# Kernel optimization log

Hardware: AMD Instinct MI355X
Metric: run time of the kernel (lower is better)

The kernel has to match this reference:

```python
import jax, jax.numpy as jnp
import numpy as np

N, E, F_IN, H, G, A, OUT = 50000, 800000, 128, 256, 64, 8, 1


def _lin(k, fi, fo):
    s = 1.0 / np.sqrt(fi)
    kw, kb = jax.random.split(k)
    W = jax.random.uniform(kw, (fi, fo), jnp.float32, -s, s)
    b = jax.random.uniform(kb, (fo,), jnp.float32, -s, s)
    return W, b


def setup_inputs() -> dict:
    key = jax.random.key(0)
    ks = jax.random.split(key, 12)
    x = jax.random.normal(ks[0], (N, F_IN), jnp.float32)
    edge_index = jax.random.randint(ks[1], (2, E), 0, N, dtype=jnp.int64)
    batch = jnp.sort(jax.random.randint(ks[2], (N,), 0, G, dtype=jnp.int64))
    graph_attr = jax.random.normal(ks[3], (G, A), jnp.float32)
    W1, b1 = _lin(ks[4], F_IN, H)
    W2, b2 = _lin(ks[5], H, H)
    W3, b3 = _lin(ks[6], H, H)
    fcW1, fcb1 = _lin(ks[7], H + A, H)
    fcW2, fcb2 = _lin(ks[8], H, OUT)
    ones = jnp.ones((H,), jnp.float32)
    zeros = jnp.zeros((H,), jnp.float32)
    return dict(x=x, graph_attr=graph_attr, edge_index=edge_index, batch=batch,
                W1=W1, b1=b1, W2=W2, b2=b2, W3=W3, b3=b3,
                g1=ones, be1=zeros, g2=ones, be2=zeros, g3=ones, be3=zeros,
                fcW1=fcW1, fcb1=fcb1, fcW2=fcW2, fcb2=fcb2)


def gcn_conv(x, W, b, src, dst, n):
    # PyG GCNConv: add self-loops, symmetric normalization, xW then scatter-add
    xw = x @ W  # [N, H]
    loop = jnp.arange(n)
    src2 = jnp.concatenate([src, loop])
    dst2 = jnp.concatenate([dst, loop])
    deg = jnp.zeros((n,), xw.dtype).at[dst2].add(1.0)
    dinv = jnp.where(deg > 0, jax.lax.rsqrt(deg), 0.0)
    norm = dinv[src2] * dinv[dst2]  # [E+N]
    out = jnp.zeros((n, xw.shape[1]), xw.dtype).at[dst2].add(xw[src2] * norm[:, None])
    return out + b


def layer_norm(x, g, b, eps=1e-5):
    m = x.mean(-1, keepdims=True)
    v = ((x - m) ** 2).mean(-1, keepdims=True)
    return (x - m) * jax.lax.rsqrt(v + eps) * g + b


def reference(x, graph_attr, edge_index, batch,
              W1, b1, W2, b2, W3, b3,
              g1, be1, g2, be2, g3, be3,
              fcW1, fcb1, fcW2, fcb2):
    src, dst = edge_index[0], edge_index[1]
    h = jax.nn.relu(layer_norm(gcn_conv(x, W1, b1, src, dst, N), g1, be1))
    h = jax.nn.relu(layer_norm(gcn_conv(h, W2, b2, src, dst, N), g2, be2))
    h = jax.nn.relu(layer_norm(gcn_conv(h, W3, b3, src, dst, N), g3, be3))
    # global mean pool over graph ids
    sums = jax.ops.segment_sum(h, batch, num_segments=G)
    cnts = jax.ops.segment_sum(jnp.ones((N,), h.dtype), batch, num_segments=G)
    pooled = sums / jnp.maximum(cnts, 1.0)[:, None]  # [G, H]
    z = jnp.concatenate([pooled, graph_attr.reshape(-1, A)], axis=1)
    z = jax.nn.relu(z @ fcW1 + fcb1)
    return z @ fcW2 + fcb2  # [G, OUT]
```

## Files before the change

kernel.cpp:

```cpp
#include <hip/hip_runtime.h>
#include <hip/hip_bf16.h>

#define N_NODES 50000
#define N_EDGES 800000
#define F_IN    128
#define H_DIM   256
#define G_NUM   64
#define A_DIM   8

typedef __attribute__((ext_vector_type(8))) short short8v;
typedef __attribute__((ext_vector_type(4))) float float4v;
typedef __attribute__((ext_vector_type(2))) float float2v;

__device__ __forceinline__ float b2f(unsigned short u) {
    return __uint_as_float(((unsigned int)u) << 16);
}
__device__ __forceinline__ unsigned short f2b(float v) {
    return __hip_bfloat16_raw(__float2bfloat16(v)).x;
}
__device__ __forceinline__ unsigned char f2fp8(float v) {
    return (unsigned char)(__builtin_amdgcn_cvt_pk_fp8_f32(v, v, 0, false) & 0xff);
}
__device__ __forceinline__ unsigned int pack2(float a, float b) {
    return (unsigned int)f2b(a) | ((unsigned int)f2b(b) << 16);
}
__device__ __forceinline__ void accadd16(float2v* a, uint4 v) {
    a[0] += __builtin_amdgcn_cvt_pk_f32_fp8((int)v.x, false);
    a[1] += __builtin_amdgcn_cvt_pk_f32_fp8((int)v.x, true);
    a[2] += __builtin_amdgcn_cvt_pk_f32_fp8((int)v.y, false);
    a[3] += __builtin_amdgcn_cvt_pk_f32_fp8((int)v.y, true);
    a[4] += __builtin_amdgcn_cvt_pk_f32_fp8((int)v.z, false);
    a[5] += __builtin_amdgcn_cvt_pk_f32_fp8((int)v.z, true);
    a[6] += __builtin_amdgcn_cvt_pk_f32_fp8((int)v.w, false);
    a[7] += __builtin_amdgcn_cvt_pk_f32_fp8((int)v.w, true);
}


__global__ void init_kernel(const int* __restrict__ dst, int* __restrict__ indeg,
                            unsigned short* __restrict__ eloc,
                            const float4* __restrict__ x, uint2* __restrict__ xb,
                            const float* __restrict__ W1, unsigned short* __restrict__ Wt1,
                            const float* __restrict__ W2, unsigned short* __restrict__ Wt2,
                            const float* __restrict__ W3, unsigned short* __restrict__ Wt3) {
    const int EB = (N_EDGES + 255) / 256;
    const int n_x4 = N_NODES * F_IN / 4;
    const int n_w1 = F_IN * H_DIM;
    const int n_w2 = H_DIM * H_DIM;
    int b = blockIdx.x, t = threadIdx.x;
    if (b < EB) {
        int i = b * 256 + t;
        if (i < N_EDGES)
            eloc[i] = (unsigned short)atomicAdd(&indeg[dst[i]], 1);
        return;
    }
    int i = (b - EB) * 256 + t;
    if (i < n_x4) {
        float4 v = x[i];
        uint2 o;
        o.x = pack2(v.x, v.y);
        o.y = pack2(v.z, v.w);
        xb[i] = o;
    } else {
        int j = i - n_x4;
        if (j < n_w1) {
            int k = j / H_DIM, n = j % H_DIM;
            Wt1[(size_t)n * F_IN + k] = f2b(W1[j]);
        } else if (j < n_w1 + n_w2) {
            int j2 = j - n_w1;
            int k = j2 / H_DIM, n = j2 % H_DIM;
            Wt2[(size_t)n * H_DIM + k] = f2b(W2[j2]);
        } else if (j < n_w1 + 2 * n_w2) {
            int j3 = j - n_w1 - n_w2;
            int k = j3 / H_DIM, n = j3 % H_DIM;
            Wt3[(size_t)n * H_DIM + k] = f2b(W3[j3]);
        }
    }
}


__global__ __launch_bounds__(256) void scan1_kernel(const int* __restrict__ in,
                                                    int* __restrict__ out,
                                                    int* __restrict__ bsum,
                                                    float* __restrict__ dinv, int n) {
    __shared__ int tile[256];
    int b = blockIdx.x, t = threadIdx.x, i = b * 256 + t;
    int v = (i < n) ? in[i] : 0;
    if (i < n) dinv[i] = rsqrtf((float)v + 1.0f);
    tile[t] = v;
    __syncthreads();
    #pragma unroll
    for (int o = 1; o < 256; o <<= 1) {
        int add = (t >= o) ? tile[t - o] : 0;
        __syncthreads();
        tile[t] += add;
        __syncthreads();
    }
    if (i < n) out[i] = tile[t] - v;
    if (t == 255) bsum[b] = tile[255];
}

__global__ __launch_bounds__(256) void scan2_kernel(int* __restrict__ bsum, int nb,
                                                    const int* __restrict__ batch,
                                                    int* __restrict__ gstart,
                                                    float* __restrict__ pooled) {
    __shared__ int tile[256];
    int t = threadIdx.x;
    int v = (t < nb) ? bsum[t] : 0;
    tile[t] = v;
    __syncthreads();
    #pragma unroll
    for (int o = 1; o < 256; o <<= 1) {
        int add = (t >= o) ? tile[t - o] : 0;
        __syncthreads();
        tile[t] += add;
        __syncthreads();
    }
    if (t < nb) bsum[t] = tile[t] - v;
    if (t <= G_NUM) {
        int lo = 0, hi = N_NODES;
        while (lo < hi) {
            int mid = (lo + hi) >> 1;
            if (batch[mid] < t) lo = mid + 1; else hi = mid;
        }
        gstart[t] = lo;
    }
    for (int i = t; i < G_NUM * H_DIM; i += 256) pooled[i] = 0.f;
}

__global__ __launch_bounds__(256) void scan3_kernel(int* __restrict__ out,
                                                    const int* __restrict__ bsum, int n) {
    int i = blockIdx.x * blockDim.x + threadIdx.x;
    if (i < n) out[i] = out[i] + bsum[i >> 8];
    if (i == 0) out[n] = N_EDGES;
}


#define SK 40

__device__ __forceinline__ void gemm_body_f8(const unsigned short* __restrict__ A,
                                             const unsigned short* __restrict__ Bt,
                                             unsigned char* __restrict__ C8,
                                             const float* __restrict__ dinv,
                                             int M, int K, int bm) {
    __shared__ unsigned short As[128][SK];
    __shared__ unsigned short Bs[256][SK];
    int t = threadIdx.x;
    int wave = t >> 6, lane = t & 63;
    int wm0 = (wave & 1) * 64, wn0 = (wave >> 1) * 64;
    int l15 = lane & 15, lq = lane >> 4;
    float4v acc[4][4];
    #pragma unroll
    for (int i = 0; i < 4; i++)
        #pragma unroll
        for (int j = 0; j < 4; j++)
            acc[i][j] = (float4v){0.f, 0.f, 0.f, 0.f};

    for (int k0 = 0; k0 < K; k0 += 32) {
        {
            int row = t >> 2, koff = (t & 3) * 8;
            uint4 va = make_uint4(0u, 0u, 0u, 0u);
            if (bm + row < M)
                va = *(const uint4*)(A + (size_t)(bm + row) * K + k0 + koff);
            *(uint4*)&As[row][koff] = va;
        }
        #pragma unroll
        for (int h = 0; h < 2; h++) {
            int c = t + h * 512;
            int row = c >> 2, koff = (c & 3) * 8;
            uint4 vb = *(const uint4*)(Bt + (size_t)row * K + k0 + koff);
            *(uint4*)&Bs[row][koff] = vb;
        }
        __syncthreads();
        short8v af[4], bf[4];
        #pragma unroll
        for (int i = 0; i < 4; i++) {
            af[i] = *(const short8v*)&As[wm0 + i * 16 + l15][lq * 8];
            bf[i] = *(const short8v*)&Bs[wn0 + i * 16 + l15][lq * 8];
        }
        #pragma unroll
        for (int i = 0; i < 4; i++)
            #pragma unroll
            for (int j = 0; j < 4; j++)
                acc[i][j] = __builtin_amdgcn_mfma_f32_16x16x32_bf16(af[i], bf[j], acc[i][j], 0, 0, 0);
        __syncthreads();
    }
    #pragma unroll
    for (int i = 0; i < 4; i++) {
        #pragma unroll
        for (int r = 0; r < 4; r++) {
            int row = bm + wm0 + i * 16 + lq * 4 + r;
            if (row < M) {
                float dv = dinv[row];
                #pragma unroll
                for (int j = 0; j < 4; j++) {
                    int col = wn0 + j * 16 + l15;
                    C8[(size_t)row * H_DIM + col] = f2fp8(dv * acc[i][j][r]);
                }
            }
        }
    }
}

__global__ __launch_bounds__(512) void gemm_f8(const unsigned short* __restrict__ A,
                                               const unsigned short* __restrict__ Bt,
                                               unsigned char* __restrict__ C8,
                                               const float* __restrict__ dinv,
                                               int M, int K) {
    gemm_body_f8(A, Bt, C8, dinv, M, K, blockIdx.x * 128);
}


__global__ __launch_bounds__(512) void fuse1_kernel(const unsigned short* __restrict__ Xb,
                                                    const unsigned short* __restrict__ Wt1,
                                                    unsigned char* __restrict__ P8,
                                                    const float* __restrict__ dinv,
                                                    const int* __restrict__ src,
                                                    const int* __restrict__ dst,
                                                    const unsigned short* __restrict__ eloc,
                                                    const int* __restrict__ rowptr,
                                                    unsigned short* __restrict__ csr_src) {
    const int GB = (N_NODES + 127) / 128;
    int b = blockIdx.x;
    if (b < GB) {
        gemm_body_f8(Xb, Wt1, P8, dinv, N_NODES, F_IN, b * 128);
        return;
    }
    int i = (b - GB) * 512 + threadIdx.x;
    if (i < N_EDGES) {
        int d = dst[i];
        csr_src[rowptr[d] + (int)eloc[i]] = (unsigned short)src[i];
    }
}


template<int F, bool DO_LN>
__global__ __launch_bounds__(256) void gather_ns(const unsigned char* __restrict__ xw,
                                                 unsigned short* __restrict__ out,
                                                 const int* __restrict__ rowptr,
                                                 const unsigned short* __restrict__ csr_src,
                                                 const float* __restrict__ dinv,
                                                 const float* __restrict__ bias,
                                                 const float* __restrict__ gamma,
                                                 const float* __restrict__ beta) {
    constexpr int BPL = F / 16;
    constexpr int NF2 = BPL / 2;
    int lane = threadIdx.x & 63;
    int wave = threadIdx.x >> 6;
    int p = lane & 15;
    int gbase = lane & 48;
    int node = blockIdx.x * 16 + wave * 4 + (lane >> 4);
    int beg = rowptr[node];
    int deg = rowptr[node + 1] - beg;
    const unsigned char* xp = xw + (size_t)p * BPL;

    float2v acc2[NF2];
    #pragma unroll
    for (int k = 0; k < NF2; k++) acc2[k] = (float2v){0.f, 0.f};

    {
        uint4 v = *(const uint4*)(xp + (size_t)node * F);
        accadd16(acc2, v);
    }

    for (int b0 = 0; b0 < deg; b0 += 16) {
        int m = deg - b0; if (m > 16) m = 16;
        int sv = (p < m) ? (int)csr_src[beg + b0 + p] : 0;
        int j = 0;
        for (; j + 4 <= m; j += 4) {
            int s0 = __shfl(sv, gbase | j, 64);
            int s1 = __shfl(sv, gbase | (j + 1), 64);
            int s2 = __shfl(sv, gbase | (j + 2), 64);
            int s3 = __shfl(sv, gbase | (j + 3), 64);
            uint4 v0 = *(const uint4*)(xp + (size_t)s0 * F);
            uint4 v1 = *(const uint4*)(xp + (size_t)s1 * F);
            uint4 v2 = *(const uint4*)(xp + (size_t)s2 * F);
            uint4 v3 = *(const uint4*)(xp + (size_t)s3 * F);
            accadd16(acc2, v0); accadd16(acc2, v1);
            accadd16(acc2, v2); accadd16(acc2, v3);
        }
        for (; j < m; ++j) {
            int s0 = __shfl(sv, gbase | j, 64);
            uint4 v0 = *(const uint4*)(xp + (size_t)s0 * F);
            accadd16(acc2, v0);
        }
    }

    float d = dinv[node];
    float v[BPL];
    #pragma unroll
    for (int k = 0; k < NF2; k++) { v[2 * k] = d * acc2[k].x; v[2 * k + 1] = d * acc2[k].y; }

    if constexpr (DO_LN) {
        #pragma unroll
        for (int q = 0; q < BPL / 4; q++) {
            float4 bi = ((const float4*)bias)[p * (BPL / 4) + q];
            v[q * 4 + 0] += bi.x; v[q * 4 + 1] += bi.y;
            v[q * 4 + 2] += bi.z; v[q * 4 + 3] += bi.w;
        }
        float s = 0.f, ss = 0.f;
        #pragma unroll
        for (int k = 0; k < BPL; k++) { s += v[k]; ss += v[k] * v[k]; }
        #pragma unroll
        for (int o = 1; o < 16; o <<= 1) {
            s  += __shfl_xor(s, o, 64);
            ss += __shfl_xor(ss, o, 64);
        }
        float mn = s * (1.f / F);
        float var = ss * (1.f / F) - mn * mn;
        float rstd = rsqrtf(var + 1e-5f);
        #pragma unroll
        for (int q = 0; q < BPL / 4; q++) {
            float4 ga = ((const float4*)gamma)[p * (BPL / 4) + q];
            float4 be = ((const float4*)beta)[p * (BPL / 4) + q];
            v[q * 4 + 0] = fmaxf((v[q * 4 + 0] - mn) * rstd * ga.x + be.x, 0.f);
            v[q * 4 + 1] = fmaxf((v[q * 4 + 1] - mn) * rstd * ga.y + be.y, 0.f);
            v[q * 4 + 2] = fmaxf((v[q * 4 + 2] - mn) * rstd * ga.z + be.z, 0.f);
            v[q * 4 + 3] = fmaxf((v[q * 4 + 3] - mn) * rstd * ga.w + be.w, 0.f);
        }
    }

    unsigned short* op = out + (size_t)node * F + p * BPL;
    uint4 o0;
    o0.x = pack2(v[0], v[1]); o0.y = pack2(v[2], v[3]);
    o0.z = pack2(v[4], v[5]); o0.w = pack2(v[6], v[7]);
    *(uint4*)op = o0;
    if constexpr (F == 256) {
        uint4 o1;
        o1.x = pack2(v[8],  v[9]);  o1.y = pack2(v[10], v[11]);
        o1.z = pack2(v[12], v[13]); o1.w = pack2(v[14], v[15]);
        *(uint4*)(op + 8) = o1;
    }
}


__global__ __launch_bounds__(128) void pool_kernel(const unsigned int* __restrict__ h32,
                                                   const int* __restrict__ batch,
                                                   float* __restrict__ pooled, int n) {
    int t = threadIdx.x;
    int start = blockIdx.x * 64;
    int end = min(start + 64, n);
    if (start >= n) return;
    int cur = batch[start];
    float a0 = 0.f, a1 = 0.f;
    for (int i = start; i < end; ++i) {
        int g = batch[i];
        if (g != cur) {
            atomicAdd(&pooled[(size_t)cur * H_DIM + 2 * t], a0);
            atomicAdd(&pooled[(size_t)cur * H_DIM + 2 * t + 1], a1);
            a0 = a1 = 0.f;
            cur = g;
        }
        unsigned int u = h32[(size_t)i * (H_DIM / 2) + t];
        a0 += b2f((unsigned short)(u & 0xffffu));
        a1 += b2f((unsigned short)(u >> 16));
    }
    atomicAdd(&pooled[(size_t)cur * H_DIM + 2 * t], a0);
    atomicAdd(&pooled[(size_t)cur * H_DIM + 2 * t + 1], a1);
}


__global__ __launch_bounds__(256) void fc_kernel(const float* __restrict__ pooled,
                                                 const int* __restrict__ gstart,
                                                 const float* __restrict__ gattr,
                                                 const float* __restrict__ fcW1,
                                                 const float* __restrict__ fcb1,
                                                 const float* __restrict__ fcW2,
                                                 const float* __restrict__ fcb2,
                                                 float* __restrict__ out) {
    __shared__ float zc[H_DIM + A_DIM];
    __shared__ float z1[H_DIM];
    int g = blockIdx.x, t = threadIdx.x;
    int c_i = gstart[g + 1] - gstart[g];
    float c = (float)(c_i > 1 ? c_i : 1);
    zc[t] = pooled[(size_t)g * H_DIM + t] / c;
    if (t < A_DIM) zc[H_DIM + t] = gattr[g * A_DIM + t];
    __syncthreads();
    float s = fcb1[t];
    for (int k = 0; k < H_DIM + A_DIM; k++)
        s += zc[k] * fcW1[(size_t)k * H_DIM + t];
    z1[t] = fmaxf(s, 0.f) * fcW2[t];
    __syncthreads();
    for (int off = 128; off; off >>= 1) {
        if (t < off) z1[t] += z1[t + off];
        __syncthreads();
    }
    if (t == 0) out[g] = z1[0] + fcb2[0];
}


extern "C" void kernel_launch(void* const* d_in, const int* in_sizes, int n_in,
                              void* d_out, int out_size, void* d_ws, size_t ws_size,
                              hipStream_t stream) {
    const float* x     = (const float*)d_in[0];
    const float* gattr = (const float*)d_in[1];
    const int*   ei    = (const int*)d_in[2];
    const int*   batch = (const int*)d_in[3];
    const float* W1 = (const float*)d_in[4];  const float* b1 = (const float*)d_in[5];
    const float* W2 = (const float*)d_in[6];  const float* b2 = (const float*)d_in[7];
    const float* W3 = (const float*)d_in[8];  const float* b3 = (const float*)d_in[9];
    const float* g1 = (const float*)d_in[10]; const float* be1 = (const float*)d_in[11];
    const float* g2 = (const float*)d_in[12]; const float* be2 = (const float*)d_in[13];
    const float* g3 = (const float*)d_in[14]; const float* be3 = (const float*)d_in[15];
    const float* fcW1 = (const float*)d_in[16]; const float* fcb1 = (const float*)d_in[17];
    const float* fcW2 = (const float*)d_in[18]; const float* fcb2 = (const float*)d_in[19];
    float* out = (float*)d_out;

    char* w = (char*)d_ws;
    unsigned char*  Pb8 = (unsigned char*)w;  w += (size_t)N_NODES * H_DIM;
    unsigned short* Hb  = (unsigned short*)w; w += (size_t)N_NODES * H_DIM * 2;
    unsigned short* Xb  = (unsigned short*)w; w += (size_t)N_NODES * F_IN * 2;
    unsigned short* Wt1 = (unsigned short*)w; w += (size_t)H_DIM * F_IN * 2;
    unsigned short* Wt2 = (unsigned short*)w; w += (size_t)H_DIM * H_DIM * 2;
    unsigned short* Wt3 = (unsigned short*)w; w += (size_t)H_DIM * H_DIM * 2;
    float* dinv   = (float*)w; w += (size_t)N_NODES * 4;
    float* pooled = (float*)w; w += (size_t)G_NUM * H_DIM * 4;
    int* indeg    = (int*)w;   w += (size_t)N_NODES * 4;
    int* rowptr   = (int*)w;   w += (size_t)(N_NODES + 4) * 4;
    unsigned short* eloc    = (unsigned short*)w; w += (size_t)N_EDGES * 2;
    unsigned short* csr_src = (unsigned short*)w; w += (size_t)N_EDGES * 2;
    int* gstart   = (int*)w;   w += (size_t)(G_NUM + 1) * 4;
    int* bsum     = (int*)w;   w += (size_t)256 * 4;

    const int* srcp = ei;
    const int* dstp = ei + N_EDGES;
    const int n_sblk = (N_NODES + 255) / 256;

    hipMemsetAsync(indeg, 0, (size_t)N_NODES * sizeof(int), stream);
    {
        const int EB = (N_EDGES + 255) / 256;
        int conv_tot = N_NODES * F_IN / 4 + F_IN * H_DIM + 2 * H_DIM * H_DIM;
        int CB = (conv_tot + 255) / 256;
        init_kernel<<<EB + CB, 256, 0, stream>>>(dstp, indeg, eloc, (const float4*)x,
                                                 (uint2*)Xb, W1, Wt1, W2, Wt2, W3, Wt3);
    }
    scan1_kernel<<<n_sblk, 256, 0, stream>>>(indeg, rowptr, bsum, dinv, N_NODES);
    scan2_kernel<<<1, 256, 0, stream>>>(bsum, n_sblk, batch, gstart, pooled);
    scan3_kernel<<<n_sblk, 256, 0, stream>>>(rowptr, bsum, N_NODES);

    int gemm_blocks = (N_NODES + 127) / 128;
    int gather_blocks = N_NODES / 16;

    {
        const int PB = (N_EDGES + 511) / 512;
        fuse1_kernel<<<gemm_blocks + PB, 512, 0, stream>>>(Xb, Wt1, Pb8, dinv,
                                                           srcp, dstp, eloc, rowptr, csr_src);
    }

    gather_ns<H_DIM, true><<<gather_blocks, 256, 0, stream>>>(Pb8, Hb, rowptr, csr_src, dinv,
                                                              b1, g1, be1);
    gemm_f8<<<gemm_blocks, 512, 0, stream>>>(Hb, Wt2, Pb8, dinv, N_NODES, H_DIM);
    gather_ns<H_DIM, true><<<gather_blocks, 256, 0, stream>>>(Pb8, Hb, rowptr, csr_src, dinv,
                                                              b2, g2, be2);
    gemm_f8<<<gemm_blocks, 512, 0, stream>>>(Hb, Wt3, Pb8, dinv, N_NODES, H_DIM);
    gather_ns<H_DIM, true><<<gather_blocks, 256, 0, stream>>>(Pb8, Hb, rowptr, csr_src, dinv,
                                                              b3, g3, be3);

    pool_kernel<<<(N_NODES + 63) / 64, 128, 0, stream>>>((const unsigned int*)Hb, batch, pooled, N_NODES);
    fc_kernel<<<G_NUM, 256, 0, stream>>>(pooled, gstart, gattr, fcW1, fcb1, fcW2, fcb2, out);
}
```

Before: 367.3 us.

## Fuse layer-1 GEMM into degree-count kernel and defer dinv scaling

The first-layer X·W1 GEMM now runs inside the initial degree-counting kernel, converting fp32 x and W1 to bf16 on the fly. This removes the separate Xb/Wt1 conversion buffers and their round trip through memory. Because dinv is not yet known at that point, the GEMM writes an unscaled bf16 result. A new kernel then scales it by dinv and packs it to fp8, running alongside the CSR fill. The cost is an extra bf16 write/read of the N×H intermediate, plus strided, uncoalesced W1 loads repeated in every GEMM block.

```diff
diff --git a/kernel.cpp b/kernel.cpp
--- a/kernel.cpp
+++ b/kernel.cpp
@@ -35,45 +35,107 @@
     a[7] += __builtin_amdgcn_cvt_pk_f32_fp8((int)v.w, true);
 }
 
-
-__global__ void init_kernel(const int* __restrict__ dst, int* __restrict__ indeg,
-                            unsigned short* __restrict__ eloc,
-                            const float4* __restrict__ x, uint2* __restrict__ xb,
-                            const float* __restrict__ W1, unsigned short* __restrict__ Wt1,
-                            const float* __restrict__ W2, unsigned short* __restrict__ Wt2,
-                            const float* __restrict__ W3, unsigned short* __restrict__ Wt3) {
-    const int EB = (N_EDGES + 255) / 256;
-    const int n_x4 = N_NODES * F_IN / 4;
-    const int n_w1 = F_IN * H_DIM;
-    const int n_w2 = H_DIM * H_DIM;
+#define SK 40
+
+
+__global__ __launch_bounds__(512) void fuseA_kernel(const int* __restrict__ dst,
+                                                    int* __restrict__ indeg,
+                                                    unsigned short* __restrict__ eloc,
+                                                    const float* __restrict__ x,
+                                                    const float* __restrict__ W1,
+                                                    unsigned short* __restrict__ Hb,
+                                                    const float* __restrict__ W2,
+                                                    unsigned short* __restrict__ Wt2,
+                                                    const float* __restrict__ W3,
+                                                    unsigned short* __restrict__ Wt3) {
+    const int EB = (N_EDGES + 511) / 512;
+    const int GB = (N_NODES + 127) / 128;
     int b = blockIdx.x, t = threadIdx.x;
     if (b < EB) {
-        int i = b * 256 + t;
+        int i = b * 512 + t;
         if (i < N_EDGES)
             eloc[i] = (unsigned short)atomicAdd(&indeg[dst[i]], 1);
         return;
     }
-    int i = (b - EB) * 256 + t;
-    if (i < n_x4) {
-        float4 v = x[i];
-        uint2 o;
-        o.x = pack2(v.x, v.y);
-        o.y = pack2(v.z, v.w);
-        xb[i] = o;
-    } else {
-        int j = i - n_x4;
-        if (j < n_w1) {
-            int k = j / H_DIM, n = j % H_DIM;
-            Wt1[(size_t)n * F_IN + k] = f2b(W1[j]);
-        } else if (j < n_w1 + n_w2) {
-            int j2 = j - n_w1;
-            int k = j2 / H_DIM, n = j2 % H_DIM;
-            Wt2[(size_t)n * H_DIM + k] = f2b(W2[j2]);
-        } else if (j < n_w1 + 2 * n_w2) {
-            int j3 = j - n_w1 - n_w2;
-            int k = j3 / H_DIM, n = j3 % H_DIM;
-            Wt3[(size_t)n * H_DIM + k] = f2b(W3[j3]);
-        }
+    b -= EB;
+    if (b < GB) {
+        __shared__ unsigned short As[128][SK];
+        __shared__ unsigned short Bs[256][SK];
+        int wave = t >> 6, lane = t & 63;
+        int wm0 = (wave & 1) * 64, wn0 = (wave >> 1) * 64;
+        int bm = b * 128;
+        int l15 = lane & 15, lq = lane >> 4;
+        float4v acc[4][4];
+        #pragma unroll
+        for (int i = 0; i < 4; i++)
+            #pragma unroll
+            for (int j = 0; j < 4; j++)
+                acc[i][j] = (float4v){0.f, 0.f, 0.f, 0.f};
+
+        for (int k0 = 0; k0 < F_IN; k0 += 32) {
+            {
+                int row = t >> 2, koff = (t & 3) * 8;
+                short8v tmp = (short8v){0,0,0,0,0,0,0,0};
+                if (bm + row < N_NODES) {
+                    const float* xp = x + (size_t)(bm + row) * F_IN + k0 + koff;
+                    float4 a0 = *(const float4*)xp;
+                    float4 a1 = *(const float4*)(xp + 4);
+                    tmp[0] = (short)f2b(a0.x); tmp[1] = (short)f2b(a0.y);
+                    tmp[2] = (short)f2b(a0.z); tmp[3] = (short)f2b(a0.w);
+                    tmp[4] = (short)f2b(a1.x); tmp[5] = (short)f2b(a1.y);
+                    tmp[6] = (short)f2b(a1.z); tmp[7] = (short)f2b(a1.w);
+                }
+                *(short8v*)&As[row][koff] = tmp;
+            }
+            #pragma unroll
+            for (int h = 0; h < 2; h++) {
+                int c = t + h * 512;
+                int n = c >> 2, koff = (c & 3) * 8;
+                short8v tmp;
+                #pragma unroll
+                for (int kk = 0; kk < 8; kk++)
+                    tmp[kk] = (short)f2b(W1[(size_t)(k0 + koff + kk) * H_DIM + n]);
+                *(short8v*)&Bs[n][koff] = tmp;
+            }
+            __syncthreads();
+            short8v af[4], bf[4];
+            #pragma unroll
+            for (int i = 0; i < 4; i++) {
+                af[i] = *(const short8v*)&As[wm0 + i * 16 + l15][lq * 8];
+                bf[i] = *(const short8v*)&Bs[wn0 + i * 16 + l15][lq * 8];
+            }
+            #pragma unroll
+            for (int i = 0; i < 4; i++)
+                #pragma unroll
+                for (int j = 0; j < 4; j++)
+                    acc[i][j] = __builtin_amdgcn_mfma_f32_16x16x32_bf16(af[i], bf[j], acc[i][j], 0, 0, 0);
+            __syncthreads();
+        }
+        #pragma unroll
+        for (int i = 0; i < 4; i++) {
+            #pragma unroll
+            for (int r = 0; r < 4; r++) {
+                int row = bm + wm0 + i * 16 + lq * 4 + r;
+                if (row < N_NODES) {
+                    #pragma unroll
+                    for (int j = 0; j < 4; j++) {
+                        int col = wn0 + j * 16 + l15;
+                        Hb[(size_t)row * H_DIM + col] = f2b(acc[i][j][r]);
+                    }
+                }
+            }
+        }
+        return;
+    }
+    b -= GB;
+    int i = b * 512 + t;
+    if (i < H_DIM * H_DIM) {
+        int k = i >> 8, n = i & 255;
+        Wt2[(size_t)n * H_DIM + k] = f2b(W2[i]);
+    } else if (i < 2 * H_DIM * H_DIM) {
+        int j = i - H_DIM * H_DIM;
+        int k = j >> 8, n = j & 255;
+        Wt3[(size_t)n * H_DIM + k] = f2b(W3[j]);
     }
 }
 
@@ -135,7 +197,44 @@
 }
 
 
-#define SK 40
+__global__ __launch_bounds__(512) void fuseB_kernel(const int* __restrict__ src,
+                                                    const int* __restrict__ dst,
+                                                    const unsigned short* __restrict__ eloc,
+                                                    const int* __restrict__ rowptr,
+                                                    unsigned short* __restrict__ csr_src,
+                                                    const uint4* __restrict__ Hb4,
+                                                    const float* __restrict__ dinv,
+                                                    uint2* __restrict__ P8) {
+    const int PB = (N_EDGES + 511) / 512;
+    int b = blockIdx.x, t = threadIdx.x;
+    if (b < PB) {
+        int i = b * 512 + t;
+        if (i < N_EDGES) {
+            int d = dst[i];
+            csr_src[rowptr[d] + (int)eloc[i]] = (unsigned short)src[i];
+        }
+        return;
+    }
+    int i = (b - PB) * 512 + t;
+    if (i < N_NODES * (H_DIM / 8)) {
+        float dv = dinv[i >> 5];
+        uint4 hv = Hb4[i];
+        float f0 = b2f((unsigned short)(hv.x & 0xffffu)) * dv;
+        float f1 = b2f((unsigned short)(hv.x >> 16)) * dv;
+        float f2 = b2f((unsigned short)(hv.y & 0xffffu)) * dv;
+        float f3 = b2f((unsigned short)(hv.y >> 16)) * dv;
+        float f4 = b2f((unsigned short)(hv.z & 0xffffu)) * dv;
+        float f5 = b2f((unsigned short)(hv.z >> 16)) * dv;
+        float f6 = b2f((unsigned short)(hv.w & 0xffffu)) * dv;
+        float f7 = b2f((unsigned short)(hv.w >> 16)) * dv;
+        unsigned int lo = (unsigned int)__builtin_amdgcn_cvt_pk_fp8_f32(f0, f1, 0, false);
+        lo = (unsigned int)__builtin_amdgcn_cvt_pk_fp8_f32(f2, f3, (int)lo, true);
+        unsigned int hi = (unsigned int)__builtin_amdgcn_cvt_pk_fp8_f32(f4, f5, 0, false);
+        hi = (unsigned int)__builtin_amdgcn_cvt_pk_fp8_f32(f6, f7, (int)hi, true);
+        P8[i] = make_uint2(lo, hi);
+    }
+}
+
 
 __device__ __forceinline__ void gemm_body_f8(const unsigned short* __restrict__ A,
                                              const unsigned short* __restrict__ Bt,
@@ -207,29 +306,6 @@
                                                const float* __restrict__ dinv,
                                                int M, int K) {
     gemm_body_f8(A, Bt, C8, dinv, M, K, blockIdx.x * 128);
-}
-
-
-__global__ __launch_bounds__(512) void fuse1_kernel(const unsigned short* __restrict__ Xb,
-                                                    const unsigned short* __restrict__ Wt1,
-                                                    unsigned char* __restrict__ P8,
-                                                    const float* __restrict__ dinv,
-                                                    const int* __restrict__ src,
-                                                    const int* __restrict__ dst,
-                                                    const unsigned short* __restrict__ eloc,
-                                                    const int* __restrict__ rowptr,
-                                                    unsigned short* __restrict__ csr_src) {
-    const int GB = (N_NODES + 127) / 128;
-    int b = blockIdx.x;
-    if (b < GB) {
-        gemm_body_f8(Xb, Wt1, P8, dinv, N_NODES, F_IN, b * 128);
-        return;
-    }
-    int i = (b - GB) * 512 + threadIdx.x;
-    if (i < N_EDGES) {
-        int d = dst[i];
-        csr_src[rowptr[d] + (int)eloc[i]] = (unsigned short)src[i];
-    }
 }
 
 
@@ -408,8 +484,6 @@
     char* w = (char*)d_ws;
     unsigned char*  Pb8 = (unsigned char*)w;  w += (size_t)N_NODES * H_DIM;
     unsigned short* Hb  = (unsigned short*)w; w += (size_t)N_NODES * H_DIM * 2;
-    unsigned short* Xb  = (unsigned short*)w; w += (size_t)N_NODES * F_IN * 2;
-    unsigned short* Wt1 = (unsigned short*)w; w += (size_t)H_DIM * F_IN * 2;
     unsigned short* Wt2 = (unsigned short*)w; w += (size_t)H_DIM * H_DIM * 2;
     unsigned short* Wt3 = (unsigned short*)w; w += (size_t)H_DIM * H_DIM * 2;
     float* dinv   = (float*)w; w += (size_t)N_NODES * 4;
@@ -427,24 +501,25 @@
 
     hipMemsetAsync(indeg, 0, (size_t)N_NODES * sizeof(int), stream);
     {
-        const int EB = (N_EDGES + 255) / 256;
-        int conv_tot = N_NODES * F_IN / 4 + F_IN * H_DIM + 2 * H_DIM * H_DIM;
-        int CB = (conv_tot + 255) / 256;
-        init_kernel<<<EB + CB, 256, 0, stream>>>(dstp, indeg, eloc, (const float4*)x,
-                                                 (uint2*)Xb, W1, Wt1, W2, Wt2, W3, Wt3);
+        const int EB = (N_EDGES + 511) / 512;
+        const int GB = (N_NODES + 127) / 128;
+        const int WB = (2 * H_DIM * H_DIM + 511) / 512;
+        fuseA_kernel<<<EB + GB + WB, 512, 0, stream>>>(dstp, indeg, eloc, x, W1, Hb,
+                                                       W2, Wt2, W3, Wt3);
     }
     scan1_kernel<<<n_sblk, 256, 0, stream>>>(indeg, rowptr, bsum, dinv, N_NODES);
     scan2_kernel<<<1, 256, 0, stream>>>(bsum, n_sblk, batch, gstart, pooled);
     scan3_kernel<<<n_sblk, 256, 0, stream>>>(rowptr, bsum, N_NODES);
 
+    {
+        const int PB = (N_EDGES + 511) / 512;
+        const int RB = (N_NODES * (H_DIM / 8) + 511) / 512;
+        fuseB_kernel<<<PB + RB, 512, 0, stream>>>(srcp, dstp, eloc, rowptr, csr_src,
+                                                  (const uint4*)Hb, dinv, (uint2*)Pb8);
+    }
+
     int gemm_blocks = (N_NODES + 127) / 128;
     int gather_blocks = N_NODES / 16;
-
-    {
-        const int PB = (N_EDGES + 511) / 512;
-        fuse1_kernel<<<gemm_blocks + PB, 512, 0, stream>>>(Xb, Wt1, Pb8, dinv,
-                                                           srcp, dstp, eloc, rowptr, csr_src);
-    }
 
     gather_ns<H_DIM, true><<<gather_blocks, 256, 0, stream>>>(Pb8, Hb, rowptr, csr_src, dinv,
                                                               b1, g1, be1);
```

Measured after the change: 373.9 us. About the same (+1.8%).
